# Kernel tuning notes

Hardware: AMD Instinct MI355X
Metric: run time of the kernel (lower is better)

## Reference

```python
import jax, jax.numpy as jnp
import numpy as np

N = 100000
IN_CH = 128
HID = 16
HEADS = 8
OUT_CH = 16
E = 1600000
NEG_SLOPE = 0.2


def glorot(key, shape, fan_in, fan_out):
    lim = jnp.sqrt(6.0 / (fan_in + fan_out)).astype(jnp.float32)
    return jax.random.uniform(key, shape, jnp.float32, -lim, lim)


def setup_inputs() -> dict:
    key = jax.random.key(0)
    ks = jax.random.split(key, 10)
    x = jax.random.normal(ks[0], (N, IN_CH), jnp.float32)
    edge_index = jax.random.randint(ks[1], (2, E), 0, N, jnp.int32)
    # layer 1: GATConv(IN_CH, HID, heads=8), concat=True
    W1 = glorot(ks[2], (IN_CH, HEADS * HID), IN_CH, HEADS * HID)
    att_src1 = glorot(ks[3], (HEADS, HID), HID, 1)
    att_dst1 = glorot(ks[4], (HEADS, HID), HID, 1)
    b1 = jnp.zeros((HEADS * HID,), jnp.float32)
    # layer 2: GATConv(HID*8, OUT_CH, heads=1)
    W2 = glorot(ks[5], (HEADS * HID, OUT_CH), HEADS * HID, OUT_CH)
    att_src2 = glorot(ks[6], (1, OUT_CH), OUT_CH, 1)
    att_dst2 = glorot(ks[7], (1, OUT_CH), OUT_CH, 1)
    b2 = jnp.zeros((OUT_CH,), jnp.float32)
    return {"x": x, "edge_index": edge_index, "W1": W1, "att_src1": att_src1,
            "att_dst1": att_dst1, "b1": b1, "W2": W2, "att_src2": att_src2,
            "att_dst2": att_dst2, "b2": b2}


def gat_layer(x, src, tgt, W, a_src, a_dst, bias, heads, ch, n):
    # h: [N, H, C]
    h = (x @ W).reshape(n, heads, ch)
    alpha_s = jnp.sum(h * a_src[None], axis=-1)  # [N, H]
    alpha_d = jnp.sum(h * a_dst[None], axis=-1)  # [N, H]
    # per-edge attention logit (message flows src -> tgt)
    e = jax.nn.leaky_relu(alpha_s[src] + alpha_d[tgt], NEG_SLOPE)  # [E, H]
    # segment softmax over target node neighborhoods (stable)
    m = jax.ops.segment_max(e, tgt, num_segments=n)  # [N, H]
    e = jnp.exp(e - m[tgt])
    denom = jax.ops.segment_sum(e, tgt, num_segments=n)
    alpha = e / (denom[tgt] + 1e-16)  # [E, H]
    # weighted scatter-add of source features
    out = jax.ops.segment_sum(h[src] * alpha[:, :, None], tgt, num_segments=n)
    return out.reshape(n, heads * ch) + bias


def reference(x, edge_index, W1, att_src1, att_dst1, b1, W2, att_src2, att_dst2, b2):
    n = x.shape[0]
    loops = jnp.arange(n, dtype=edge_index.dtype)
    src = jnp.concatenate([edge_index[0], loops])
    tgt = jnp.concatenate([edge_index[1], loops])
    h = gat_layer(x, src, tgt, W1, att_src1, att_dst1, b1, HEADS, HID, n)
    h = jax.nn.elu(h)
    out = gat_layer(h, src, tgt, W2, att_src2, att_dst2, b2, 1, OUT_CH, n)
    return out
```

## Files before the change

### kernel.cpp

```cpp
#include <hip/hip_runtime.h>
#include <hip/hip_fp16.h>
#include <math.h>

#define IN_CH 128
#define HEADS 8
#define HID 16
#define OUT_CH 16
#define NEG 0.2f
#define NPB 256
#define MAXBUCK 400
#define AST 136

__device__ __forceinline__ float lrelu(float x){ return x > 0.f ? x : NEG * x; }

typedef _Float16 half8 __attribute__((ext_vector_type(8)));
typedef float    f32x4 __attribute__((ext_vector_type(4)));

__global__ __launch_bounds__(256) void k_bhist(const int* __restrict__ tgt, int E, int nbuck, int epb,
                                               int* __restrict__ bcnt){
    __shared__ int hist[MAXBUCK];
    int tid = threadIdx.x;
    for (int i = tid; i < nbuck; i += 256) hist[i] = 0;
    __syncthreads();
    int start = blockIdx.x * epb, end = min(start + epb, E);
    for (int e = start + tid; e < end; e += 256) atomicAdd(&hist[tgt[e] >> 8], 1);
    __syncthreads();
    for (int i = tid; i < nbuck; i += 256) if (hist[i]) atomicAdd(&bcnt[i], hist[i]);
}

__global__ void k_bscan(const int* __restrict__ bcnt, int nbuck, int E,
                        int* __restrict__ boffs, int* __restrict__ bcur){
    __shared__ int s[512];
    int t = threadIdx.x;
    int v = (t < nbuck) ? bcnt[t] : 0;
    int orig = v;
    s[t] = v; __syncthreads();
    for (int off = 1; off < 512; off <<= 1){
        int u = (t >= off) ? s[t - off] : 0;
        __syncthreads();
        v += u; s[t] = v; __syncthreads();
    }
    if (t < nbuck){ boffs[t] = v - orig; bcur[t] = v - orig; }
    if (t == 0) boffs[nbuck] = E;
}

__global__ __launch_bounds__(256) void k_bscatter(const int* __restrict__ ei, int E, int nbuck, int epb,
                                                  int* __restrict__ bcur, int2* __restrict__ ebuck){
    __shared__ int hist[MAXBUCK];
    __shared__ int base[MAXBUCK];
    int tid = threadIdx.x;
    for (int i = tid; i < nbuck; i += 256) hist[i] = 0;
    __syncthreads();
    int start = blockIdx.x * epb, end = min(start + epb, E);
    for (int e = start + tid; e < end; e += 256) atomicAdd(&hist[ei[E + e] >> 8], 1);
    __syncthreads();
    for (int i = tid; i < nbuck; i += 256){
        base[i] = hist[i] ? atomicAdd(&bcur[i], hist[i]) : 0;
        hist[i] = 0;
    }
    __syncthreads();
    for (int e = start + tid; e < end; e += 256){
        int s = ei[e], t = ei[E + e];
        int b = t >> 8;
        int r = atomicAdd(&hist[b], 1);
        ebuck[base[b] + r] = make_int2(s, t);
    }
}

__global__ __launch_bounds__(256) void k_csr(const int2* __restrict__ ebuck, const int* __restrict__ boffs,
                                             int N, int E,
                                             int* __restrict__ offs, int* __restrict__ esrc){
    __shared__ int cnt[256];
    __shared__ int sscan[256];
    __shared__ int wcur[256];
    int b = blockIdx.x;
    int tid = threadIdx.x;
    int n0 = b * 256;
    int nn = min(256, N - n0);
    cnt[tid] = (tid < nn) ? 1 : 0;
    __syncthreads();
    int e0 = boffs[b], e1 = boffs[b + 1];
    for (int e = e0 + tid; e < e1; e += 256) atomicAdd(&cnt[ebuck[e].y & 255], 1);
    __syncthreads();
    int v = cnt[tid], orig = v;
    sscan[tid] = v; __syncthreads();
    for (int off = 1; off < 256; off <<= 1){
        int u = (tid >= off) ? sscan[tid - off] : 0;
        __syncthreads();
        v += u; sscan[tid] = v; __syncthreads();
    }
    int excl = v - orig;
    int gbase = e0 + n0;
    if (tid < nn){
        offs[n0 + tid] = gbase + excl;
        esrc[gbase + excl] = n0 + tid;
    }
    wcur[tid] = excl + 1;
    __syncthreads();
    for (int e = e0 + tid; e < e1; e += 256){
        int2 p = ebuck[e];
        int r = atomicAdd(&wcur[p.y & 255], 1);
        esrc[gbase + r] = p.x;
    }
    if (b == 0 && tid == 0) offs[N] = E + N;
}

__global__ __launch_bounds__(256) void k_gemm1(const float* __restrict__ x, const float* __restrict__ W1,
                                               __half* __restrict__ h1, int N){
    __shared__ _Float16 sA[64*AST];
    __shared__ _Float16 sB[128*AST];
    int tid = threadIdx.x;
    for (int i = tid; i < 128*128; i += 256){
        int k = i >> 7, c = i & 127;
        sB[c*AST + k] = (_Float16)W1[i];
    }
    int row0 = blockIdx.x * 64;
    #pragma unroll
    for (int i = 0; i < 8; ++i){
        int q = i*256 + tid;
        int r = q >> 5, seg = q & 31;
        float4 v = make_float4(0.f,0.f,0.f,0.f);
        if (row0 + r < N) v = *(const float4*)(x + (size_t)(row0+r)*128 + seg*4);
        _Float16* dst = &sA[r*AST + seg*4];
        dst[0]=(_Float16)v.x; dst[1]=(_Float16)v.y; dst[2]=(_Float16)v.z; dst[3]=(_Float16)v.w;
    }
    __syncthreads();
    int wave = tid >> 6, lane = tid & 63;
    int m = lane & 15, quad = lane >> 4;
    int rbase = wave * 16;
    f32x4 acc[8] = {};
    #pragma unroll
    for (int kc = 0; kc < 4; ++kc){
        int kb = kc*32 + quad*8;
        half8 a = *(half8*)(&sA[(rbase + m)*AST + kb]);
        #pragma unroll
        for (int t = 0; t < 8; ++t){
            half8 b = *(half8*)(&sB[(t*16 + m)*AST + kb]);
            acc[t] = __builtin_amdgcn_mfma_f32_16x16x32_f16(a, b, acc[t], 0, 0, 0);
        }
    }
    #pragma unroll
    for (int t = 0; t < 8; ++t){
        #pragma unroll
        for (int j = 0; j < 4; ++j){
            int r = row0 + rbase + quad*4 + j;
            if (r < N) h1[(size_t)r*128 + t*16 + m] = __float2half(acc[t][j]);
        }
    }
}

struct H8 { __half2 v[8]; };

__global__ void k_alpha1(const __half2* __restrict__ h1h, const float* __restrict__ asrc, const float* __restrict__ adst,
                         float* __restrict__ as1, float* __restrict__ ad1, int N){
    int idx = blockIdx.x*blockDim.x + threadIdx.x;
    if (idx >= N*HEADS) return;
    int h = idx & 7;
    int n = idx >> 3;
    H8 blk = *(const H8*)(h1h + (size_t)n*64 + h*8);
    const float2* sp = (const float2*)(asrc + h*16);
    const float2* dp = (const float2*)(adst + h*16);
    float ss = 0.f, dd = 0.f;
    #pragma unroll
    for (int j = 0; j < 8; ++j){
        float2 v = __half22float2(blk.v[j]);
        float2 a = sp[j], b = dp[j];
        ss += v.x*a.x + v.y*a.y;
        dd += v.x*b.x + v.y*b.y;
    }
    as1[idx] = ss; ad1[idx] = dd;
}

__global__ __launch_bounds__(256) void k_agg1(const __half2* __restrict__ h1h, const float* __restrict__ as1,
                                              const float* __restrict__ ad1,
                                              const int* __restrict__ offs, const int* __restrict__ esrc,
                                              const float* __restrict__ b1, __half2* __restrict__ hl2h, int N){
    int n = blockIdx.x*4 + (threadIdx.x >> 6);
    if (n >= N) return;
    int l = threadIdx.x & 63;
    int h = l >> 3;
    float adh = ad1[n*8 + h];
    int e0 = offs[n], e1 = offs[n+1];

    float2 acc0 = make_float2(0.f,0.f), acc1 = make_float2(0.f,0.f);
    float2 acc2 = make_float2(0.f,0.f), acc3 = make_float2(0.f,0.f);
    float den0 = 0.f, den1 = 0.f, den2 = 0.f, den3 = 0.f;
    int e = e0;
    for (; e + 4 <= e1; e += 4){
        int s0 = esrc[e], s1 = esrc[e+1], s2 = esrc[e+2], s3 = esrc[e+3];
        float a0 = as1[s0*8 + h], a1 = as1[s1*8 + h];
        float a2 = as1[s2*8 + h], a3 = as1[s3*8 + h];
        float2 h0 = __half22float2(h1h[(size_t)s0*64 + l]);
        float2 h1v = __half22float2(h1h[(size_t)s1*64 + l]);
        float2 h2v = __half22float2(h1h[(size_t)s2*64 + l]);
        float2 h3v = __half22float2(h1h[(size_t)s3*64 + l]);
        float w0 = __expf(lrelu(a0 + adh));
        float w1 = __expf(lrelu(a1 + adh));
        float w2 = __expf(lrelu(a2 + adh));
        float w3 = __expf(lrelu(a3 + adh));
        den0 += w0; den1 += w1; den2 += w2; den3 += w3;
        acc0.x += w0*h0.x;  acc0.y += w0*h0.y;
        acc1.x += w1*h1v.x; acc1.y += w1*h1v.y;
        acc2.x += w2*h2v.x; acc2.y += w2*h2v.y;
        acc3.x += w3*h3v.x; acc3.y += w3*h3v.y;
    }
    for (; e < e1; ++e){
        int s0 = esrc[e];
        float w0 = __expf(lrelu(as1[s0*8 + h] + adh));
        float2 h0 = __half22float2(h1h[(size_t)s0*64 + l]);
        den0 += w0;
        acc0.x += w0*h0.x; acc0.y += w0*h0.y;
    }
    float rd = 1.f / (den0 + den1 + den2 + den3 + 1e-16f);
    float2 bb = ((const float2*)b1)[l];
    float vx = (acc0.x + acc1.x + acc2.x + acc3.x)*rd + bb.x;
    float vy = (acc0.y + acc1.y + acc2.y + acc3.y)*rd + bb.y;
    vx = vx > 0.f ? vx : expm1f(vx);
    vy = vy > 0.f ? vy : expm1f(vy);
    hl2h[(size_t)n*64 + l] = __floats2half2_rn(vx, vy);
}

#define FMA4(acc, a, b) { acc.x += (a)*(b).x; acc.y += (a)*(b).y; acc.z += (a)*(b).z; acc.w += (a)*(b).w; }

__global__ __launch_bounds__(256) void k_gemm2(const __half2* __restrict__ hl2h, const float* __restrict__ W2,
                                               const float* __restrict__ asrc2, const float* __restrict__ adst2,
                                               float* __restrict__ h2, float* __restrict__ as2, float* __restrict__ ad2,
                                               int N){
    __shared__ float sX[64*132];
    __shared__ float sW2[128*16];
    int tid = threadIdx.x;
    for (int i = tid; i < 128*16; i += 256) sW2[i] = W2[i];
    int row0 = blockIdx.x * 64;
    #pragma unroll
    for (int i = 0; i < 4; ++i){
        int q = i*256 + tid;
        int r = q >> 4, seg = q & 15;
        float4 raw = make_float4(0.f,0.f,0.f,0.f);
        if (row0 + r < N) raw = ((const float4*)(hl2h + (size_t)(row0+r)*64))[seg];
        const __half2* hp = (const __half2*)&raw;
        float* dst = &sX[r*132 + seg*8];
        #pragma unroll
        for (int j = 0; j < 4; ++j){
            float2 f = __half22float2(hp[j]);
            dst[2*j] = f.x; dst[2*j+1] = f.y;
        }
    }
    __syncthreads();
    int nd = tid >> 2;
    int cq = tid & 3, c0 = cq*4;
    int n = row0 + nd;
    float4 acc = make_float4(0.f,0.f,0.f,0.f);
    #pragma unroll 4
    for (int k4 = 0; k4 < 32; ++k4){
        float4 a  = *(const float4*)(&sX[nd*132 + k4*4]);
        float4 w0 = *(const float4*)(&sW2[(k4*4+0)*16 + c0]);
        float4 w1 = *(const float4*)(&sW2[(k4*4+1)*16 + c0]);
        float4 w2 = *(const float4*)(&sW2[(k4*4+2)*16 + c0]);
        float4 w3 = *(const float4*)(&sW2[(k4*4+3)*16 + c0]);
        FMA4(acc, a.x, w0); FMA4(acc, a.y, w1); FMA4(acc, a.z, w2); FMA4(acc, a.w, w3);
    }
    float ps = acc.x*asrc2[c0] + acc.y*asrc2[c0+1] + acc.z*asrc2[c0+2] + acc.w*asrc2[c0+3];
    float pd = acc.x*adst2[c0] + acc.y*adst2[c0+1] + acc.z*adst2[c0+2] + acc.w*adst2[c0+3];
    ps += __shfl_xor(ps, 1); ps += __shfl_xor(ps, 2);
    pd += __shfl_xor(pd, 1); pd += __shfl_xor(pd, 2);
    if (n < N){
        *(float4*)(&h2[(size_t)n*16 + c0]) = acc;
        if (cq == 0){ as2[n] = ps; ad2[n] = pd; }
    }
}

__global__ __launch_bounds__(256) void k_agg2(const float* __restrict__ h2, const float* __restrict__ as2v,
                                              const float* __restrict__ ad2v,
                                              const int* __restrict__ offs, const int* __restrict__ esrc,
                                              const float* __restrict__ b2, float* __restrict__ out, int N){
    int n = blockIdx.x*4 + (threadIdx.x >> 6);
    if (n >= N) return;
    int l = threadIdx.x & 63;
    int e0 = offs[n], e1 = offs[n+1];
    float ad = ad2v[n];
    int eo = l >> 4, c = l & 15;
    float acc = 0.f, den = 0.f;
    for (int e = e0 + eo; e < e1; e += 4){
        int s = esrc[e];
        float w = __expf(lrelu(as2v[s] + ad));
        den += w;
        acc += w * h2[(size_t)s*16 + c];
    }
    acc += __shfl_xor(acc, 16); den += __shfl_xor(den, 16);
    acc += __shfl_xor(acc, 32); den += __shfl_xor(den, 32);
    if (eo == 0) out[(size_t)n*16 + c] = acc / (den + 1e-16f) + b2[c];
}

extern "C" void kernel_launch(void* const* d_in, const int* in_sizes, int n_in,
                              void* d_out, int out_size, void* d_ws, size_t ws_size,
                              hipStream_t stream){
    const float* x     = (const float*)d_in[0];
    const int*   ei    = (const int*)  d_in[1];
    const float* W1    = (const float*)d_in[2];
    const float* asrc1 = (const float*)d_in[3];
    const float* adst1 = (const float*)d_in[4];
    const float* b1    = (const float*)d_in[5];
    const float* W2    = (const float*)d_in[6];
    const float* asrc2 = (const float*)d_in[7];
    const float* adst2 = (const float*)d_in[8];
    const float* b2    = (const float*)d_in[9];
    float* out = (float*)d_out;

    const int N = in_sizes[0] / IN_CH;
    const int E = in_sizes[1] / 2;
    const int ETOT = E + N;
    const int NBUCK = (N + NPB - 1) / NPB;

    char* p = (char*)d_ws;
    auto alloc = [&](size_t bytes) -> char* {
        char* r = p; p += (bytes + 255) & ~(size_t)255; return r;
    };
    __half2* h1h  = (__half2*)alloc((size_t)N * 64 * 4);
    __half2* hl2h = (__half2*)alloc((size_t)N * 64 * 4);
    float* as1   = (float*)alloc((size_t)N * 8 * 4);
    float* ad1   = (float*)alloc((size_t)N * 8 * 4);
    float* h2    = (float*)alloc((size_t)N * 16 * 4);
    float* as2   = (float*)alloc((size_t)N * 4);
    float* ad2   = (float*)alloc((size_t)N * 4);
    int*   bcnt  = (int*)  alloc((size_t)MAXBUCK * 4);
    int*   boffs = (int*)  alloc((size_t)(MAXBUCK + 1) * 4);
    int*   bcur  = (int*)  alloc((size_t)MAXBUCK * 4);
    int*   offs  = (int*)  alloc((size_t)(N + 1) * 4);
    int*   esrc  = (int*)  alloc((size_t)ETOT * 4);
    int2*  ebuck = (int2*)hl2h;

    hipMemsetAsync(bcnt, 0, (size_t)NBUCK * 4, stream);

    const int GPART = 512;
    const int epb = (E + GPART - 1) / GPART;

    k_bhist   <<<GPART, 256, 0, stream>>>(ei + E, E, NBUCK, epb, bcnt);
    k_bscan   <<<1,     512, 0, stream>>>(bcnt, NBUCK, E, boffs, bcur);
    k_bscatter<<<GPART, 256, 0, stream>>>(ei, E, NBUCK, epb, bcur, ebuck);
    k_csr     <<<NBUCK, 256, 0, stream>>>(ebuck, boffs, N, E, offs, esrc);

    k_gemm1  <<<(N + 63) / 64, 256, 0, stream>>>(x, W1, (__half*)h1h, N);
    k_alpha1 <<<(N * HEADS + 255) / 256, 256, 0, stream>>>(h1h, asrc1, adst1, as1, ad1, N);
    k_agg1   <<<(N + 3) / 4, 256, 0, stream>>>(h1h, as1, ad1, offs, esrc, b1, hl2h, N);
    k_gemm2  <<<(N + 63) / 64, 256, 0, stream>>>(hl2h, W2, asrc2, adst2, h2, as2, ad2, N);
    k_agg2   <<<(N + 3) / 4, 256, 0, stream>>>(h2, as2, ad2, offs, esrc, b2, out, N);
}
```

Before: 356.5 us.

## Process two nodes per wavefront in agg1 and store layer-2 features as fp16

The layer-1 aggregation now gives each 32-lane half-wave its own target node. Each lane loads four fp16 channels (8 bytes) per edge, and both halves loop to the larger degree with masked edges. The layer-2 projected features are written and gathered as fp16 instead of fp32, which halves the bytes gathered per edge in agg2. This trades some divergence from degree imbalance between paired nodes and added fp16 rounding error for fewer, wider memory transactions.

```diff
diff --git a/kernel.cpp b/kernel.cpp
--- a/kernel.cpp
+++ b/kernel.cpp
@@ -175,56 +175,62 @@
                                               const float* __restrict__ ad1,
                                               const int* __restrict__ offs, const int* __restrict__ esrc,
                                               const float* __restrict__ b1, __half2* __restrict__ hl2h, int N){
-    int n = blockIdx.x*4 + (threadIdx.x >> 6);
-    if (n >= N) return;
-    int l = threadIdx.x & 63;
-    int h = l >> 3;
-    float adh = ad1[n*8 + h];
-    int e0 = offs[n], e1 = offs[n+1];
-
-    float2 acc0 = make_float2(0.f,0.f), acc1 = make_float2(0.f,0.f);
-    float2 acc2 = make_float2(0.f,0.f), acc3 = make_float2(0.f,0.f);
-    float den0 = 0.f, den1 = 0.f, den2 = 0.f, den3 = 0.f;
-    int e = e0;
-    for (; e + 4 <= e1; e += 4){
-        int s0 = esrc[e], s1 = esrc[e+1], s2 = esrc[e+2], s3 = esrc[e+3];
+    int wv = threadIdx.x >> 6;
+    int l  = threadIdx.x & 63;
+    int sub = l >> 5, ll = l & 31;
+    int n = blockIdx.x*8 + wv*2 + sub;
+    bool alive = (n < N);
+    int h = ll >> 2;
+    float adh = 0.f;
+    int e0 = 0, deg = 0;
+    if (alive){
+        adh = ad1[n*8 + h];
+        e0 = offs[n];
+        deg = offs[n+1] - e0;
+    }
+    int degmax = max(deg, __shfl_xor(deg, 32));
+
+    float4 acc0 = make_float4(0.f,0.f,0.f,0.f), acc1 = make_float4(0.f,0.f,0.f,0.f);
+    float den0 = 0.f, den1 = 0.f;
+    for (int i = 0; i < degmax; i += 2){
+        bool v0 = i < deg, v1 = (i+1) < deg;
+        int i0 = e0 + (v0 ? i   : 0);
+        int i1 = e0 + (v1 ? i+1 : 0);
+        int s0 = esrc[i0], s1 = esrc[i1];
         float a0 = as1[s0*8 + h], a1 = as1[s1*8 + h];
-        float a2 = as1[s2*8 + h], a3 = as1[s3*8 + h];
-        float2 h0 = __half22float2(h1h[(size_t)s0*64 + l]);
-        float2 h1v = __half22float2(h1h[(size_t)s1*64 + l]);
-        float2 h2v = __half22float2(h1h[(size_t)s2*64 + l]);
-        float2 h3v = __half22float2(h1h[(size_t)s3*64 + l]);
-        float w0 = __expf(lrelu(a0 + adh));
-        float w1 = __expf(lrelu(a1 + adh));
-        float w2 = __expf(lrelu(a2 + adh));
-        float w3 = __expf(lrelu(a3 + adh));
-        den0 += w0; den1 += w1; den2 += w2; den3 += w3;
-        acc0.x += w0*h0.x;  acc0.y += w0*h0.y;
-        acc1.x += w1*h1v.x; acc1.y += w1*h1v.y;
-        acc2.x += w2*h2v.x; acc2.y += w2*h2v.y;
-        acc3.x += w3*h3v.x; acc3.y += w3*h3v.y;
-    }
-    for (; e < e1; ++e){
-        int s0 = esrc[e];
-        float w0 = __expf(lrelu(as1[s0*8 + h] + adh));
-        float2 h0 = __half22float2(h1h[(size_t)s0*64 + l]);
-        den0 += w0;
-        acc0.x += w0*h0.x; acc0.y += w0*h0.y;
-    }
-    float rd = 1.f / (den0 + den1 + den2 + den3 + 1e-16f);
-    float2 bb = ((const float2*)b1)[l];
-    float vx = (acc0.x + acc1.x + acc2.x + acc3.x)*rd + bb.x;
-    float vy = (acc0.y + acc1.y + acc2.y + acc3.y)*rd + bb.y;
-    vx = vx > 0.f ? vx : expm1f(vx);
-    vy = vy > 0.f ? vy : expm1f(vy);
-    hl2h[(size_t)n*64 + l] = __floats2half2_rn(vx, vy);
+        float2 p0 = *(const float2*)(h1h + (size_t)s0*64 + ll*2);
+        float2 p1 = *(const float2*)(h1h + (size_t)s1*64 + ll*2);
+        float w0 = v0 ? __expf(lrelu(a0 + adh)) : 0.f;
+        float w1 = v1 ? __expf(lrelu(a1 + adh)) : 0.f;
+        float2 f0a = __half22float2(*(__half2*)&p0.x), f0b = __half22float2(*(__half2*)&p0.y);
+        float2 f1a = __half22float2(*(__half2*)&p1.x), f1b = __half22float2(*(__half2*)&p1.y);
+        den0 += w0; den1 += w1;
+        acc0.x += w0*f0a.x; acc0.y += w0*f0a.y; acc0.z += w0*f0b.x; acc0.w += w0*f0b.y;
+        acc1.x += w1*f1a.x; acc1.y += w1*f1a.y; acc1.z += w1*f1b.x; acc1.w += w1*f1b.y;
+    }
+    if (!alive) return;
+    float rd = 1.f / (den0 + den1 + 1e-16f);
+    float4 bb = *(const float4*)(b1 + ll*4);
+    float o0 = (acc0.x + acc1.x)*rd + bb.x;
+    float o1 = (acc0.y + acc1.y)*rd + bb.y;
+    float o2 = (acc0.z + acc1.z)*rd + bb.z;
+    float o3 = (acc0.w + acc1.w)*rd + bb.w;
+    o0 = o0 > 0.f ? o0 : expm1f(o0);
+    o1 = o1 > 0.f ? o1 : expm1f(o1);
+    o2 = o2 > 0.f ? o2 : expm1f(o2);
+    o3 = o3 > 0.f ? o3 : expm1f(o3);
+    __half2 q0 = __floats2half2_rn(o0, o1);
+    __half2 q1 = __floats2half2_rn(o2, o3);
+    float2 ov;
+    *(__half2*)&ov.x = q0; *(__half2*)&ov.y = q1;
+    *(float2*)(hl2h + (size_t)n*64 + ll*2) = ov;
 }
 
 #define FMA4(acc, a, b) { acc.x += (a)*(b).x; acc.y += (a)*(b).y; acc.z += (a)*(b).z; acc.w += (a)*(b).w; }
 
 __global__ __launch_bounds__(256) void k_gemm2(const __half2* __restrict__ hl2h, const float* __restrict__ W2,
                                                const float* __restrict__ asrc2, const float* __restrict__ adst2,
-                                               float* __restrict__ h2, float* __restrict__ as2, float* __restrict__ ad2,
+                                               __half2* __restrict__ h2h, float* __restrict__ as2, float* __restrict__ ad2,
                                                int N){
     __shared__ float sX[64*132];
     __shared__ float sW2[128*16];
@@ -264,12 +270,16 @@
     ps += __shfl_xor(ps, 1); ps += __shfl_xor(ps, 2);
     pd += __shfl_xor(pd, 1); pd += __shfl_xor(pd, 2);
     if (n < N){
-        *(float4*)(&h2[(size_t)n*16 + c0]) = acc;
+        __half2 p0 = __floats2half2_rn(acc.x, acc.y);
+        __half2 p1 = __floats2half2_rn(acc.z, acc.w);
+        float2 ov;
+        *(__half2*)&ov.x = p0; *(__half2*)&ov.y = p1;
+        *(float2*)(h2h + (size_t)n*8 + cq*2) = ov;
         if (cq == 0){ as2[n] = ps; ad2[n] = pd; }
     }
 }
 
-__global__ __launch_bounds__(256) void k_agg2(const float* __restrict__ h2, const float* __restrict__ as2v,
+__global__ __launch_bounds__(256) void k_agg2(const __half* __restrict__ h2x, const float* __restrict__ as2v,
                                               const float* __restrict__ ad2v,
                                               const int* __restrict__ offs, const int* __restrict__ esrc,
                                               const float* __restrict__ b2, float* __restrict__ out, int N){
@@ -284,7 +294,7 @@
         int s = esrc[e];
         float w = __expf(lrelu(as2v[s] + ad));
         den += w;
-        acc += w * h2[(size_t)s*16 + c];
+        acc += w * __half2float(h2x[(size_t)s*16 + c]);
     }
     acc += __shfl_xor(acc, 16); den += __shfl_xor(den, 16);
     acc += __shfl_xor(acc, 32); den += __shfl_xor(den, 32);
@@ -319,7 +329,7 @@
     __half2* hl2h = (__half2*)alloc((size_t)N * 64 * 4);
     float* as1   = (float*)alloc((size_t)N * 8 * 4);
     float* ad1   = (float*)alloc((size_t)N * 8 * 4);
-    float* h2    = (float*)alloc((size_t)N * 16 * 4);
+    __half2* h2h = (__half2*)alloc((size_t)N * 8 * 4);
     float* as2   = (float*)alloc((size_t)N * 4);
     float* ad2   = (float*)alloc((size_t)N * 4);
     int*   bcnt  = (int*)  alloc((size_t)MAXBUCK * 4);
@@ -341,7 +351,7 @@
 
     k_gemm1  <<<(N + 63) / 64, 256, 0, stream>>>(x, W1, (__half*)h1h, N);
     k_alpha1 <<<(N * HEADS + 255) / 256, 256, 0, stream>>>(h1h, asrc1, adst1, as1, ad1, N);
-    k_agg1   <<<(N + 3) / 4, 256, 0, stream>>>(h1h, as1, ad1, offs, esrc, b1, hl2h, N);
-    k_gemm2  <<<(N + 63) / 64, 256, 0, stream>>>(hl2h, W2, asrc2, adst2, h2, as2, ad2, N);
-    k_agg2   <<<(N + 3) / 4, 256, 0, stream>>>(h2, as2, ad2, offs, esrc, b2, out, N);
-}
+    k_agg1   <<<(N + 7) / 8, 256, 0, stream>>>(h1h, as1, ad1, offs, esrc, b1, hl2h, N);
+    k_gemm2  <<<(N + 63) / 64, 256, 0, stream>>>(hl2h, W2, asrc2, adst2, h2h, as2, ad2, N);
+    k_agg2   <<<(N + 3) / 4, 256, 0, stream>>>((const __half*)h2h, as2, ad2, offs, esrc, b2, out, N);
+}
```

Result: no change. 350.5 us (-1.7%).
